# Performance work log

Measured on AMD Instinct MI355X. Metric: run time of the kernel, lower is better.

The kernel has to match this reference:

```python
import jax, jax.numpy as jnp
import numpy as np

B, T, D, H = 32, 4096, 512, 512


def setup_inputs() -> dict:
    key = jax.random.key(0)
    ks = jax.random.split(key, 8)
    s = 1.0 / np.sqrt(D)
    return {
        "hidden_state": jax.random.normal(ks[0], (B, D), jnp.float32),
        "encoder_outputs": jax.random.normal(ks[1], (B, T, D), jnp.float32),
        "W": jax.random.normal(ks[2], (D, H), jnp.float32) * s,
        "U": jax.random.normal(ks[3], (D, H), jnp.float32) * s,
        "V": jax.random.normal(ks[4], (H,), jnp.float32) * s,
        "bias": jnp.zeros((H,), jnp.float32),
        "Wa": jax.random.normal(ks[5], (H, H), jnp.float32) * (1.0 / np.sqrt(H)),
        "ba": jnp.zeros((H,), jnp.float32),
    }


def reference(hidden_state, encoder_outputs, W, U, V, bias, Wa, ba):
    # dens1: [B,1,H] ; dens2: [B,T,H]
    dens1 = jnp.einsum('bd,dh->bh', hidden_state, W)[:, None, :]
    dens2 = jnp.einsum('btd,dh->bth', encoder_outputs, U)
    pre = dens1 + dens2 + bias                       # [B,T,H]
    tanh_ = jnp.tanh(jnp.einsum('bth,hk->btk', pre, Wa) + ba)  # extra Dense(tanh)
    cij = jnp.einsum('bth,h->bt', tanh_, V)          # [B,T]
    alphas = jax.nn.softmax(cij, axis=-1)            # [B,T]
    output = jnp.einsum('btd,bt->bd', encoder_outputs, alphas)  # weighted sum
    return output, alphas
```

## Files before the change

kernel.cpp:

```cpp
#include <hip/hip_runtime.h>
#include <hip/hip_bf16.h>


#define BB 32
#define TT 4096
#define DD 512
#define HH 512

typedef short s16x8 __attribute__((ext_vector_type(8)));
typedef float f32x4 __attribute__((ext_vector_type(4)));

union FU { float f; unsigned u; };

static __device__ __forceinline__ unsigned pack_bf16_trunc(float a, float b) {
    FU ua, ub; ua.f = a; ub.f = b;
    return (ua.u >> 16) | (ub.u & 0xffff0000u);
}

static __device__ __forceinline__ unsigned short f2bf_rne(float x) {
    FU v; v.f = x;
    unsigned u = v.u;
    u = u + 0x7fffu + ((u >> 16) & 1u);
    return (unsigned short)(u >> 16);
}

static __device__ __forceinline__ float tanh_fast(float x) {
    float e = __expf(2.0f * x);
    return 1.0f - 2.0f * __builtin_amdgcn_rcpf(e + 1.0f);
}

__global__ void k_prep(const float* __restrict__ hs, const float* __restrict__ W,
                       const float* __restrict__ bias, const float* __restrict__ Wa,
                       const float* __restrict__ ba, const float* __restrict__ U,
                       float* __restrict__ cvec, unsigned short* __restrict__ Btf) {
    int bi = blockIdx.x;
    int tid = threadIdx.x;
    __shared__ float sm[8 * DD];
    if (bi < 32) {
        int b = bi;
        float* hsb = sm;
        float* gs = sm + DD;
        hsb[tid] = hs[b * DD + tid];
        hsb[tid + 256] = hs[b * DD + tid + 256];
        __syncthreads();
        float a0 = bias[tid], a1 = bias[tid + 256];
        #pragma unroll 4
        for (int d = 0; d < DD; ++d) {
            float h = hsb[d];
            a0 = fmaf(h, W[(size_t)d * HH + tid], a0);
            a1 = fmaf(h, W[(size_t)d * HH + tid + 256], a1);
        }
        gs[tid] = a0;
        gs[tid + 256] = a1;
        __syncthreads();
        float c0 = ba[tid], c1 = ba[tid + 256];
        #pragma unroll 4
        for (int h = 0; h < HH; ++h) {
            float g = gs[h];
            c0 = fmaf(g, Wa[(size_t)h * HH + tid], c0);
            c1 = fmaf(g, Wa[(size_t)h * HH + tid + 256], c1);
        }
        cvec[b * HH + tid] = c0;
        cvec[b * HH + tid + 256] = c1;
    } else {
        int d0 = (bi - 32) * 8;
        float (*Us)[DD] = (float (*)[DD])sm;
        #pragma unroll
        for (int i = 0; i < 16; ++i) {
            int idx = i * 256 + tid;
            Us[idx >> 9][idx & 511] = U[(size_t)(d0 + (idx >> 9)) * HH + (idx & 511)];
        }
        __syncthreads();
        float acc[8][2] = {};
        #pragma unroll 2
        for (int h = 0; h < DD; ++h) {
            float w0 = Wa[(size_t)h * HH + tid];
            float w1 = Wa[(size_t)h * HH + 256 + tid];
            #pragma unroll
            for (int dd = 0; dd < 8; ++dd) {
                float u = Us[dd][h];
                acc[dd][0] = fmaf(u, w0, acc[dd][0]);
                acc[dd][1] = fmaf(u, w1, acc[dd][1]);
            }
        }
        int fk = d0 >> 5, qq = (d0 >> 3) & 3;
        #pragma unroll
        for (int half = 0; half < 2; ++half) {
            int n = tid + half * 256;
            unsigned short tmp[8];
            #pragma unroll
            for (int dd = 0; dd < 8; ++dd) tmp[dd] = f2bf_rne(acc[dd][half]);
            size_t base = ((size_t)((n >> 4) * 16 + fk) * 64 + (n & 15) + (qq << 4)) * 8;
            *(uint4*)&Btf[base] = *(const uint4*)tmp;
        }
    }
}

__global__ void __launch_bounds__(256, 3) k_gemm_tanh(
    const float* __restrict__ e, const unsigned short* __restrict__ Btf,
    const float* __restrict__ cvec, const float* __restrict__ V,
    float* __restrict__ cijp) {
    int tid = threadIdx.x;
    int nh = blockIdx.x & 1;
    int m0 = (blockIdx.x >> 1) * 64;
    int lane = tid & 63, w = tid >> 6;
    int lcol = lane & 15, q = lane >> 4;

    __shared__ __align__(16) unsigned short As[64 * 256];

    const float* Abase = e + (size_t)m0 * DD;
    f32x4 acc[4][4] = {};
    s16x8 bfr[2][4];
    const unsigned short* Bw = Btf + (size_t)(nh * 16 + w * 4) * 16 * 64 * 8;

    #pragma unroll
    for (int half = 0; half < 2; ++half) {
        if (half) __syncthreads();
        #pragma unroll 2
        for (int it = 0; it < 8; ++it) {
            int idx = it * 256 + tid;
            int m = idx >> 5, c2 = idx & 31;
            const float* p = Abase + (size_t)m * DD + half * 256 + c2 * 8;
            float4 v0 = *(const float4*)p;
            float4 v1 = *(const float4*)(p + 4);
            uint4 u;
            u.x = pack_bf16_trunc(v0.x, v0.y);
            u.y = pack_bf16_trunc(v0.z, v0.w);
            u.z = pack_bf16_trunc(v1.x, v1.y);
            u.w = pack_bf16_trunc(v1.z, v1.w);
            *(uint4*)&As[(m * 32 + (c2 ^ (m & 31))) * 8] = u;
        }
        __syncthreads();
        #pragma unroll
        for (int j = 0; j < 4; ++j)
            bfr[0][j] = *(const s16x8*)(Bw +
                ((size_t)(j * 16 + half * 8) * 64 + lane) * 8);
        #pragma unroll
        for (int kk = 0; kk < 8; ++kk) {
            int cur = kk & 1;
            if (kk < 7) {
                #pragma unroll
                for (int j = 0; j < 4; ++j)
                    bfr[cur ^ 1][j] = *(const s16x8*)(Bw +
                        ((size_t)(j * 16 + half * 8 + kk + 1) * 64 + lane) * 8);
            }
            s16x8 af[4];
            #pragma unroll
            for (int i = 0; i < 4; ++i) {
                int m = i * 16 + lcol;
                af[i] = *(const s16x8*)&As[(m * 32 + ((kk * 4 + q) ^ (m & 31))) * 8];
            }
            #pragma unroll
            for (int i = 0; i < 4; ++i)
                #pragma unroll
                for (int j = 0; j < 4; ++j)
                    acc[i][j] = __builtin_amdgcn_mfma_f32_16x16x32_bf16(
                        af[i], bfr[cur][j], acc[i][j], 0, 0, 0);
        }
    }

    __syncthreads();
    float* red = (float*)As;
    int b = m0 >> 12;
    float cvv[4], Vv[4];
    #pragma unroll
    for (int j = 0; j < 4; ++j) {
        int h = nh * 256 + w * 64 + j * 16 + lcol;
        cvv[j] = cvec[b * HH + h];
        Vv[j] = V[h];
    }
    #pragma unroll
    for (int i = 0; i < 4; ++i) {
        #pragma unroll
        for (int r = 0; r < 4; ++r) {
            float s = 0.0f;
            #pragma unroll
            for (int j = 0; j < 4; ++j)
                s = fmaf(tanh_fast(acc[i][j][r] + cvv[j]), Vv[j], s);
            s += __shfl_xor(s, 1);
            s += __shfl_xor(s, 2);
            s += __shfl_xor(s, 4);
            s += __shfl_xor(s, 8);
            if (lcol == 0)
                red[w * 64 + i * 16 + q * 4 + r] = s;
        }
    }
    __syncthreads();
    if (tid < 64)
        cijp[(size_t)nh * (BB * TT) + m0 + tid] =
            red[tid] + red[64 + tid] + red[128 + tid] + red[192 + tid];
}

__global__ void k_softmax(const float* __restrict__ cijp, float* __restrict__ alphas) {
    int b = blockIdx.x, tid = threadIdx.x;
    const float* r0 = cijp + (size_t)b * TT;
    const float* r1 = r0 + (size_t)BB * TT;
    __shared__ float red[4];
    __shared__ float rowbuf[TT / 256 * 256];
    float m = -1e30f;
    for (int t = tid; t < TT; t += 256) m = fmaxf(m, r0[t] + r1[t]);
    #pragma unroll
    for (int o = 1; o < 64; o <<= 1) m = fmaxf(m, __shfl_xor(m, o));
    if ((tid & 63) == 0) red[tid >> 6] = m;
    __syncthreads();
    m = fmaxf(fmaxf(red[0], red[1]), fmaxf(red[2], red[3]));
    __syncthreads();
    float sum = 0.0f;
    for (int t = tid; t < TT; t += 256) {
        float v = __expf(r0[t] + r1[t] - m);
        rowbuf[t & 4095] = v;
        sum += v;
    }
    #pragma unroll
    for (int o = 1; o < 64; o <<= 1) sum += __shfl_xor(sum, o);
    if ((tid & 63) == 0) red[tid >> 6] = sum;
    __syncthreads();
    float inv = 1.0f / (red[0] + red[1] + red[2] + red[3]);
    for (int t = tid; t < TT; t += 256)
        alphas[(size_t)b * TT + t] = rowbuf[t] * inv;
}

__global__ void k_wsum(const float* __restrict__ e, const float* __restrict__ alphas,
                       float* __restrict__ pw) {
    int b = blockIdx.x >> 6;
    int chunk = blockIdx.x & 63;
    int tid = threadIdx.x;
    int half = tid >> 7, f4 = tid & 127;
    const float* base = e + (size_t)b * TT * DD + (size_t)chunk * 64 * DD + f4 * 4;
    const float* al = alphas + (size_t)b * TT + chunk * 64;
    f32x4 a0 = {0,0,0,0}, a1 = {0,0,0,0}, a2 = {0,0,0,0}, a3 = {0,0,0,0};
    for (int it = 0; it < 8; ++it) {
        int t = it * 8 + half;
        float w0 = al[t], w1 = al[t + 2], w2 = al[t + 4], w3 = al[t + 6];
        a0 += w0 * *(const f32x4*)(base + (size_t)t * DD);
        a1 += w1 * *(const f32x4*)(base + (size_t)(t + 2) * DD);
        a2 += w2 * *(const f32x4*)(base + (size_t)(t + 4) * DD);
        a3 += w3 * *(const f32x4*)(base + (size_t)(t + 6) * DD);
    }
    a0 += a1; a2 += a3; a0 += a2;
    __shared__ f32x4 red[128];
    if (half == 1) red[f4] = a0;
    __syncthreads();
    if (half == 0) {
        a0 += red[f4];
        *(f32x4*)&pw[((size_t)(b * 64 + chunk)) * DD + f4 * 4] = a0;
    }
}

__global__ void k_wred(const float* __restrict__ pw, float* __restrict__ out) {
    int b = blockIdx.x, tid = threadIdx.x;
    float2 acc = {0.0f, 0.0f};
    const float* base = pw + (size_t)b * 64 * DD;
    #pragma unroll 4
    for (int c = 0; c < 64; ++c) {
        float2 v = *(const float2*)(base + (size_t)c * DD + tid * 2);
        acc.x += v.x;
        acc.y += v.y;
    }
    *(float2*)&out[b * DD + tid * 2] = acc;
}

extern "C" void kernel_launch(void* const* d_in, const int* in_sizes, int n_in,
                              void* d_out, int out_size, void* d_ws, size_t ws_size,
                              hipStream_t stream) {
    const float* hs   = (const float*)d_in[0];
    const float* e    = (const float*)d_in[1];
    const float* W    = (const float*)d_in[2];
    const float* U    = (const float*)d_in[3];
    const float* V    = (const float*)d_in[4];
    const float* bias = (const float*)d_in[5];
    const float* Wa   = (const float*)d_in[6];
    const float* ba   = (const float*)d_in[7];

    float* out    = (float*)d_out;
    float* alphas = out + BB * DD;

    float*          cijp = (float*)d_ws;
    float*          cvec = (float*)((char*)d_ws + 1048576);
    unsigned short* Btf  = (unsigned short*)((char*)d_ws + 1114112);
    float*          pw   = (float*)((char*)d_ws + 1703936);


    k_prep<<<96, 256, 0, stream>>>(hs, W, bias, Wa, ba, U, cvec, Btf);
    k_gemm_tanh<<<4096, 256, 0, stream>>>(e, Btf, cvec, V, cijp);
    k_softmax<<<BB, 256, 0, stream>>>(cijp, alphas);
    k_wsum<<<BB * 64, 256, 0, stream>>>(e, alphas, pw);
    k_wred<<<BB, 256, 0, stream>>>(pw, out);
}
```

Measured before the change: 577.9 us.

## Pre-convert encoder outputs to bf16 and use LDS-DMA 128x128 GEMM tiles

Adds a conversion kernel that writes encoder_outputs once as bf16 to workspace. Both the tanh GEMM and the weighted-sum kernel then read the half-size copy. The GEMM is restructured into 128x128 tiles with 64-wide K steps. Both operands are staged through LDS with global_load_lds and XOR swizzling, and the transposed U·Wa weight is stored as a plain row-major bf16 matrix. The change trades an extra full read/write pass over the input for cheaper downstream reads. It also gives up register prefetch of B, and the weighted sum now uses bf16-rounded encoder values.

```diff
diff --git a/kernel.cpp b/kernel.cpp
--- a/kernel.cpp
+++ b/kernel.cpp
@@ -6,16 +6,12 @@
 #define TT 4096
 #define DD 512
 #define HH 512
+#define MM (BB * TT)
 
 typedef short s16x8 __attribute__((ext_vector_type(8)));
 typedef float f32x4 __attribute__((ext_vector_type(4)));
 
 union FU { float f; unsigned u; };
-
-static __device__ __forceinline__ unsigned pack_bf16_trunc(float a, float b) {
-    FU ua, ub; ua.f = a; ub.f = b;
-    return (ua.u >> 16) | (ub.u & 0xffff0000u);
-}
 
 static __device__ __forceinline__ unsigned short f2bf_rne(float x) {
     FU v; v.f = x;
@@ -29,10 +25,33 @@
     return 1.0f - 2.0f * __builtin_amdgcn_rcpf(e + 1.0f);
 }
 
+static __device__ __forceinline__ void gload_lds16(const void* g, void* l) {
+    __builtin_amdgcn_global_load_lds(
+        (const __attribute__((address_space(1))) unsigned int*)g,
+        (__attribute__((address_space(3))) unsigned int*)l, 16, 0, 0);
+}
+
+__global__ void k_conv(const float* __restrict__ e, unsigned short* __restrict__ ebf) {
+    size_t idx = (size_t)blockIdx.x * 256 + threadIdx.x;
+    #pragma unroll
+    for (int it = 0; it < 8; ++it) {
+        size_t g = idx + (size_t)it * 1048576;
+        const float* p = e + g * 8;
+        float4 v0 = *(const float4*)p;
+        float4 v1 = *(const float4*)(p + 4);
+        union { unsigned short us[8]; uint4 u4; } o;
+        o.us[0] = f2bf_rne(v0.x); o.us[1] = f2bf_rne(v0.y);
+        o.us[2] = f2bf_rne(v0.z); o.us[3] = f2bf_rne(v0.w);
+        o.us[4] = f2bf_rne(v1.x); o.us[5] = f2bf_rne(v1.y);
+        o.us[6] = f2bf_rne(v1.z); o.us[7] = f2bf_rne(v1.w);
+        *(uint4*)(ebf + g * 8) = o.u4;
+    }
+}
+
 __global__ void k_prep(const float* __restrict__ hs, const float* __restrict__ W,
                        const float* __restrict__ bias, const float* __restrict__ Wa,
                        const float* __restrict__ ba, const float* __restrict__ U,
-                       float* __restrict__ cvec, unsigned short* __restrict__ Btf) {
+                       float* __restrict__ cvec, unsigned short* __restrict__ UWaT) {
     int bi = blockIdx.x;
     int tid = threadIdx.x;
     __shared__ float sm[8 * DD];
@@ -83,79 +102,63 @@
                 acc[dd][1] = fmaf(u, w1, acc[dd][1]);
             }
         }
-        int fk = d0 >> 5, qq = (d0 >> 3) & 3;
-        #pragma unroll
-        for (int half = 0; half < 2; ++half) {
-            int n = tid + half * 256;
-            unsigned short tmp[8];
-            #pragma unroll
-            for (int dd = 0; dd < 8; ++dd) tmp[dd] = f2bf_rne(acc[dd][half]);
-            size_t base = ((size_t)((n >> 4) * 16 + fk) * 64 + (n & 15) + (qq << 4)) * 8;
-            *(uint4*)&Btf[base] = *(const uint4*)tmp;
-        }
-    }
-}
-
-__global__ void __launch_bounds__(256, 3) k_gemm_tanh(
-    const float* __restrict__ e, const unsigned short* __restrict__ Btf,
+        #pragma unroll
+        for (int dd = 0; dd < 8; ++dd) {
+            UWaT[(size_t)tid * DD + d0 + dd] = f2bf_rne(acc[dd][0]);
+            UWaT[(size_t)(tid + 256) * DD + d0 + dd] = f2bf_rne(acc[dd][1]);
+        }
+    }
+}
+
+__global__ void k_gemm_tanh(
+    const unsigned short* __restrict__ ebf, const unsigned short* __restrict__ Bt,
     const float* __restrict__ cvec, const float* __restrict__ V,
     float* __restrict__ cijp) {
     int tid = threadIdx.x;
-    int nh = blockIdx.x & 1;
-    int m0 = (blockIdx.x >> 1) * 64;
+    int nt = blockIdx.x & 3;
+    int m0 = (blockIdx.x >> 2) * 128;
+    int n0 = nt * 128;
     int lane = tid & 63, w = tid >> 6;
+    int wm = (w >> 1) * 64, wn = (w & 1) * 64;
     int lcol = lane & 15, q = lane >> 4;
-
-    __shared__ __align__(16) unsigned short As[64 * 256];
-
-    const float* Abase = e + (size_t)m0 * DD;
+    int rl = lane >> 3, gg = lane & 7;
+
+    __shared__ __align__(16) unsigned short As[128 * 64];
+    __shared__ __align__(16) unsigned short Bs[128 * 64];
+
     f32x4 acc[4][4] = {};
-    s16x8 bfr[2][4];
-    const unsigned short* Bw = Btf + (size_t)(nh * 16 + w * 4) * 16 * 64 * 8;
-
-    #pragma unroll
-    for (int half = 0; half < 2; ++half) {
-        if (half) __syncthreads();
-        #pragma unroll 2
-        for (int it = 0; it < 8; ++it) {
-            int idx = it * 256 + tid;
-            int m = idx >> 5, c2 = idx & 31;
-            const float* p = Abase + (size_t)m * DD + half * 256 + c2 * 8;
-            float4 v0 = *(const float4*)p;
-            float4 v1 = *(const float4*)(p + 4);
-            uint4 u;
-            u.x = pack_bf16_trunc(v0.x, v0.y);
-            u.y = pack_bf16_trunc(v0.z, v0.w);
-            u.z = pack_bf16_trunc(v1.x, v1.y);
-            u.w = pack_bf16_trunc(v1.z, v1.w);
-            *(uint4*)&As[(m * 32 + (c2 ^ (m & 31))) * 8] = u;
+
+    const unsigned short* Ab = ebf + (size_t)(m0 + w * 32 + rl) * DD + ((gg ^ rl) << 3);
+    const unsigned short* Bb = Bt + (size_t)(n0 + w * 32 + rl) * DD + ((gg ^ rl) << 3);
+
+    for (int k0 = 0; k0 < DD; k0 += 64) {
+        if (k0) __syncthreads();
+        #pragma unroll
+        for (int u = 0; u < 4; ++u) {
+            gload_lds16(Ab + (size_t)(u * 8) * DD + k0, &As[(w * 32 + u * 8) * 64]);
+            gload_lds16(Bb + (size_t)(u * 8) * DD + k0, &Bs[(w * 32 + u * 8) * 64]);
         }
         __syncthreads();
         #pragma unroll
-        for (int j = 0; j < 4; ++j)
-            bfr[0][j] = *(const s16x8*)(Bw +
-                ((size_t)(j * 16 + half * 8) * 64 + lane) * 8);
-        #pragma unroll
-        for (int kk = 0; kk < 8; ++kk) {
-            int cur = kk & 1;
-            if (kk < 7) {
-                #pragma unroll
-                for (int j = 0; j < 4; ++j)
-                    bfr[cur ^ 1][j] = *(const s16x8*)(Bw +
-                        ((size_t)(j * 16 + half * 8 + kk + 1) * 64 + lane) * 8);
+        for (int ks = 0; ks < 2; ++ks) {
+            int gk = ks * 4;
+            s16x8 af[4], bfr[4];
+            #pragma unroll
+            for (int i = 0; i < 4; ++i) {
+                int row = wm + i * 16 + lcol;
+                af[i] = *(const s16x8*)&As[(row * 8 + ((gk + q) ^ (row & 7))) * 8];
             }
-            s16x8 af[4];
-            #pragma unroll
-            for (int i = 0; i < 4; ++i) {
-                int m = i * 16 + lcol;
-                af[i] = *(const s16x8*)&As[(m * 32 + ((kk * 4 + q) ^ (m & 31))) * 8];
+            #pragma unroll
+            for (int j = 0; j < 4; ++j) {
+                int col = wn + j * 16 + lcol;
+                bfr[j] = *(const s16x8*)&Bs[(col * 8 + ((gk + q) ^ (col & 7))) * 8];
             }
             #pragma unroll
             for (int i = 0; i < 4; ++i)
                 #pragma unroll
                 for (int j = 0; j < 4; ++j)
                     acc[i][j] = __builtin_amdgcn_mfma_f32_16x16x32_bf16(
-                        af[i], bfr[cur][j], acc[i][j], 0, 0, 0);
+                        af[i], bfr[j], acc[i][j], 0, 0, 0);
         }
     }
 
@@ -165,7 +168,7 @@
     float cvv[4], Vv[4];
     #pragma unroll
     for (int j = 0; j < 4; ++j) {
-        int h = nh * 256 + w * 64 + j * 16 + lcol;
+        int h = n0 + wn + j * 16 + lcol;
         cvv[j] = cvec[b * HH + h];
         Vv[j] = V[h];
     }
@@ -186,19 +189,24 @@
         }
     }
     __syncthreads();
-    if (tid < 64)
-        cijp[(size_t)nh * (BB * TT) + m0 + tid] =
-            red[tid] + red[64 + tid] + red[128 + tid] + red[192 + tid];
+    if (tid < 128) {
+        int half = tid >> 6, row = tid & 63;
+        cijp[(size_t)nt * MM + m0 + half * 64 + row] =
+            red[(half * 2) * 64 + row] + red[(half * 2 + 1) * 64 + row];
+    }
 }
 
 __global__ void k_softmax(const float* __restrict__ cijp, float* __restrict__ alphas) {
     int b = blockIdx.x, tid = threadIdx.x;
     const float* r0 = cijp + (size_t)b * TT;
-    const float* r1 = r0 + (size_t)BB * TT;
     __shared__ float red[4];
-    __shared__ float rowbuf[TT / 256 * 256];
+    __shared__ float rowbuf[TT];
     float m = -1e30f;
-    for (int t = tid; t < TT; t += 256) m = fmaxf(m, r0[t] + r1[t]);
+    for (int t = tid; t < TT; t += 256) {
+        float v = r0[t] + r0[MM + t] + r0[2 * MM + t] + r0[3 * MM + t];
+        rowbuf[t] = v;
+        m = fmaxf(m, v);
+    }
     #pragma unroll
     for (int o = 1; o < 64; o <<= 1) m = fmaxf(m, __shfl_xor(m, o));
     if ((tid & 63) == 0) red[tid >> 6] = m;
@@ -207,8 +215,8 @@
     __syncthreads();
     float sum = 0.0f;
     for (int t = tid; t < TT; t += 256) {
-        float v = __expf(r0[t] + r1[t] - m);
-        rowbuf[t & 4095] = v;
+        float v = __expf(rowbuf[t] - m);
+        rowbuf[t] = v;
         sum += v;
     }
     #pragma unroll
@@ -220,30 +228,43 @@
         alphas[(size_t)b * TT + t] = rowbuf[t] * inv;
 }
 
-__global__ void k_wsum(const float* __restrict__ e, const float* __restrict__ alphas,
-                       float* __restrict__ pw) {
+__global__ void k_wsum(const unsigned short* __restrict__ ebf,
+                       const float* __restrict__ alphas, float* __restrict__ pw) {
     int b = blockIdx.x >> 6;
     int chunk = blockIdx.x & 63;
     int tid = threadIdx.x;
-    int half = tid >> 7, f4 = tid & 127;
-    const float* base = e + (size_t)b * TT * DD + (size_t)chunk * 64 * DD + f4 * 4;
+    int rg = tid >> 6, f8 = tid & 63;
+    const unsigned short* base =
+        ebf + (size_t)b * TT * DD + (size_t)chunk * 64 * DD + f8 * 8;
     const float* al = alphas + (size_t)b * TT + chunk * 64;
-    f32x4 a0 = {0,0,0,0}, a1 = {0,0,0,0}, a2 = {0,0,0,0}, a3 = {0,0,0,0};
-    for (int it = 0; it < 8; ++it) {
-        int t = it * 8 + half;
-        float w0 = al[t], w1 = al[t + 2], w2 = al[t + 4], w3 = al[t + 6];
-        a0 += w0 * *(const f32x4*)(base + (size_t)t * DD);
-        a1 += w1 * *(const f32x4*)(base + (size_t)(t + 2) * DD);
-        a2 += w2 * *(const f32x4*)(base + (size_t)(t + 4) * DD);
-        a3 += w3 * *(const f32x4*)(base + (size_t)(t + 6) * DD);
-    }
-    a0 += a1; a2 += a3; a0 += a2;
-    __shared__ f32x4 red[128];
-    if (half == 1) red[f4] = a0;
-    __syncthreads();
-    if (half == 0) {
-        a0 += red[f4];
-        *(f32x4*)&pw[((size_t)(b * 64 + chunk)) * DD + f4 * 4] = a0;
+    float a8[8] = {};
+    for (int it = 0; it < 16; ++it) {
+        int t = it * 4 + rg;
+        float a = al[t];
+        uint4 v = *(const uint4*)(base + (size_t)t * DD);
+        FU f;
+        f.u = v.x << 16;          a8[0] = fmaf(a, f.f, a8[0]);
+        f.u = v.x & 0xffff0000u;  a8[1] = fmaf(a, f.f, a8[1]);
+        f.u = v.y << 16;          a8[2] = fmaf(a, f.f, a8[2]);
+        f.u = v.y & 0xffff0000u;  a8[3] = fmaf(a, f.f, a8[3]);
+        f.u = v.z << 16;          a8[4] = fmaf(a, f.f, a8[4]);
+        f.u = v.z & 0xffff0000u;  a8[5] = fmaf(a, f.f, a8[5]);
+        f.u = v.w << 16;          a8[6] = fmaf(a, f.f, a8[6]);
+        f.u = v.w & 0xffff0000u;  a8[7] = fmaf(a, f.f, a8[7]);
+    }
+    __shared__ float red[3 * 512];
+    if (rg > 0) {
+        #pragma unroll
+        for (int z = 0; z < 8; ++z) red[(rg - 1) * 512 + f8 * 8 + z] = a8[z];
+    }
+    __syncthreads();
+    if (rg == 0) {
+        #pragma unroll
+        for (int z = 0; z < 8; ++z)
+            a8[z] += red[f8 * 8 + z] + red[512 + f8 * 8 + z] + red[1024 + f8 * 8 + z];
+        float* o = pw + ((size_t)(b * 64 + chunk)) * DD + f8 * 8;
+        #pragma unroll
+        for (int z = 0; z < 8; ++z) o[z] = a8[z];
     }
 }
 
@@ -276,14 +297,16 @@
     float* alphas = out + BB * DD;
 
     float*          cijp = (float*)d_ws;
-    float*          cvec = (float*)((char*)d_ws + 1048576);
-    unsigned short* Btf  = (unsigned short*)((char*)d_ws + 1114112);
-    float*          pw   = (float*)((char*)d_ws + 1703936);
-
-
-    k_prep<<<96, 256, 0, stream>>>(hs, W, bias, Wa, ba, U, cvec, Btf);
-    k_gemm_tanh<<<4096, 256, 0, stream>>>(e, Btf, cvec, V, cijp);
+    float*          cvec = (float*)((char*)d_ws + 2097152);
+    unsigned short* Bt   = (unsigned short*)((char*)d_ws + 2162688);
+    float*          pw   = (float*)((char*)d_ws + 2686976);
+    unsigned short* ebf  = (unsigned short*)((char*)d_ws + 6881280);
+
+
+    k_conv<<<4096, 256, 0, stream>>>(e, ebf);
+    k_prep<<<96, 256, 0, stream>>>(hs, W, bias, Wa, ba, U, cvec, Bt);
+    k_gemm_tanh<<<4096, 256, 0, stream>>>(ebf, Bt, cvec, V, cijp);
     k_softmax<<<BB, 256, 0, stream>>>(cijp, alphas);
-    k_wsum<<<BB * 64, 256, 0, stream>>>(e, alphas, pw);
+    k_wsum<<<BB * 64, 256, 0, stream>>>(ebf, alphas, pw);
     k_wred<<<BB, 256, 0, stream>>>(pw, out);
 }
```

Measured after the change: 609.9 us. 5.5% more time.
